# Kernel tuning notes

Hardware: AMD Instinct MI355X
Metric: run time of the kernel (lower is better)

The kernel has to match this reference:

```python
import jax, jax.numpy as jnp
import numpy as np

N_NODES = 100000
N_EDGES = 1250000
NUM_RELS = 8
D_IN, D_HID, D_OUT = 64, 64, 32


def setup_inputs() -> dict:
    key = jax.random.key(0)
    ks = jax.random.split(key, 10)
    x = jax.random.normal(ks[0], (N_NODES, D_IN), dtype=jnp.float32)
    src = jax.random.randint(ks[1], (N_EDGES,), 0, N_NODES, dtype=jnp.int32)
    dst = jax.random.randint(ks[2], (N_EDGES,), 0, N_NODES, dtype=jnp.int32)
    edge_type = jax.random.randint(ks[3], (N_EDGES,), 0, NUM_RELS, dtype=jnp.int32)
    s1 = 1.0 / np.sqrt(D_IN)
    s2 = 1.0 / np.sqrt(D_HID)
    W1 = jax.random.uniform(ks[4], (NUM_RELS, D_IN, D_HID), jnp.float32, -s1, s1)
    root1 = jax.random.uniform(ks[5], (D_IN, D_HID), jnp.float32, -s1, s1)
    b1 = jnp.zeros((D_HID,), jnp.float32)
    W2 = jax.random.uniform(ks[6], (NUM_RELS, D_HID, D_OUT), jnp.float32, -s2, s2)
    root2 = jax.random.uniform(ks[7], (D_HID, D_OUT), jnp.float32, -s2, s2)
    b2 = jnp.zeros((D_OUT,), jnp.float32)
    return {"x": x, "W1": W1, "root1": root1, "b1": b1,
            "W2": W2, "root2": root2, "b2": b2,
            "src": src, "dst": dst, "edge_type": edge_type}


def rgcn_conv(x, W, root, b, src, dst, edge_type, num_rels, num_nodes):
    # self-loop (root) transform + bias
    out = x @ root + b
    for r in range(num_rels):  # loop over small fixed relation set
        mask = (edge_type == r).astype(x.dtype)          # (E,)
        h = x @ W[r]                                      # (N, dout): transform once per relation
        msg = h[src] * mask[:, None]                      # (E, dout) gather + mask
        agg = jax.ops.segment_sum(msg, dst, num_segments=num_nodes)
        cnt = jax.ops.segment_sum(mask, dst, num_segments=num_nodes)
        out = out + agg / jnp.maximum(cnt, 1.0)[:, None]  # per-relation mean (PyG default aggr)
    return out


def reference(x, W1, root1, b1, W2, root2, b2, src, dst, edge_type):
    h = jax.nn.relu(rgcn_conv(x, W1, root1, b1, src, dst, edge_type, NUM_RELS, N_NODES))
    return rgcn_conv(h, W2, root2, b2, src, dst, edge_type, NUM_RELS, N_NODES)
```

## Files before the change

### kernel.cpp

```cpp
#include <hip/hip_runtime.h>

typedef _Float16 half8 __attribute__((ext_vector_type(8)));
typedef __attribute__((ext_vector_type(4))) float f32x4;

__device__ __forceinline__ unsigned short f2h(float f) {
    _Float16 h = (_Float16)f;
    return *(unsigned short*)&h;
}
__device__ __forceinline__ float h2f(unsigned short u) {
    _Float16 h = *(_Float16*)&u;
    return (float)h;
}


__device__ __forceinline__ void wprep_body(
    const float* __restrict__ W, const float* __restrict__ root,
    unsigned short* __restrict__ wb, int dout, int idx)
{
    int c = idx / (64 * dout);
    int rme = idx % (64 * dout);
    int kk = rme / dout;
    int j = rme % dout;
    float f = (c == 0) ? root[kk * dout + j]
                       : W[(size_t)(c - 1) * 64 * dout + kk * dout + j];
    wb[(size_t)c * dout * 72 + (size_t)j * 72 + kk] = f2h(f);
}

__global__ __launch_bounds__(256) void prep_kernel(
    const float* __restrict__ x, unsigned short* __restrict__ xh, int n8,
    const float* __restrict__ W1, const float* __restrict__ root1,
    unsigned short* __restrict__ wb1,
    const float* __restrict__ W2, const float* __restrict__ root2,
    unsigned short* __restrict__ wb2,
    int* __restrict__ hist, int nhist4)
{
    int id = blockIdx.x * 256 + threadIdx.x;
    if (id < n8) {
        const f32x4* p = (const f32x4*)(x + (size_t)id * 8);
        f32x4 u = p[0], v = p[1];
        half8 o;
#pragma unroll
        for (int j = 0; j < 4; ++j) {
            o[j] = (_Float16)u[j];
            o[j + 4] = (_Float16)v[j];
        }
        *(half8*)(xh + (size_t)id * 8) = o;
        return;
    }
    id -= n8;
    if (id < 9 * 64 * 64) { wprep_body(W1, root1, wb1, 64, id); return; }
    id -= 9 * 64 * 64;
    if (id < 9 * 64 * 32) { wprep_body(W2, root2, wb2, 32, id); return; }
    id -= 9 * 64 * 32;
    if (id < nhist4) ((int4*)hist)[id] = make_int4(0, 0, 0, 0);
}


__global__ __launch_bounds__(256) void hist8_kernel(
    const int* __restrict__ dst, const int* __restrict__ et,
    int* __restrict__ hist, int* __restrict__ rank, int E)
{
    int e = blockIdx.x * 256 + threadIdx.x;
    if (e < E) rank[e] = atomicAdd(&hist[dst[e] * 8 + et[e]], 1);
}

#define SCAN_TILE 4096
__global__ __launch_bounds__(1024) void scanA_kernel(
    const int* __restrict__ hist, int* __restrict__ bstart,
    int* __restrict__ partial, int nkeys)
{
    __shared__ int wsum[16];
    const int t = threadIdx.x;
    const int lane = t & 63, w = t >> 6;
    const int base = blockIdx.x * SCAN_TILE + t * 4;
    int v[4];
    int s = 0;
#pragma unroll
    for (int i = 0; i < 4; ++i) {
        v[i] = (base + i < nkeys) ? hist[base + i] : 0;
        s += v[i];
    }
    int inc = s;
#pragma unroll
    for (int off = 1; off < 64; off <<= 1) {
        int u = __shfl_up(inc, off);
        if (lane >= off) inc += u;
    }
    if (lane == 63) wsum[w] = inc;
    __syncthreads();
    if (w == 0 && lane < 16) {
        int ws = wsum[lane];
        int winc = ws;
#pragma unroll
        for (int off = 1; off < 16; off <<= 1) {
            int u = __shfl_up(winc, off);
            if (lane >= off) winc += u;
        }
        wsum[lane] = winc - ws;
    }
    __syncthreads();
    int run = wsum[w] + (inc - s);
    int tbase = run;
#pragma unroll
    for (int i = 0; i < 4; ++i) {
        if (base + i < nkeys) bstart[base + i] = run;
        run += v[i];
    }
    if (t == 1023) partial[blockIdx.x] = tbase + s;
}

__global__ __launch_bounds__(64) void scanB_kernel(
    const int* __restrict__ partial, int* __restrict__ pscan,
    int* __restrict__ bstart_end, int nblk)
{
    const int lane = threadIdx.x;
    int running = 0;
    for (int b = 0; b < nblk; b += 64) {
        int i = b + lane;
        int o = (i < nblk) ? partial[i] : 0;
        int v = o;
#pragma unroll
        for (int off = 1; off < 64; off <<= 1) {
            int u = __shfl_up(v, off);
            if (lane >= off) v += u;
        }
        if (i < nblk) pscan[i] = running + v - o;
        running += __shfl(v, 63);
    }
    if (lane == 0) *bstart_end = running;
}

__global__ __launch_bounds__(1024) void scanC_kernel(
    int* __restrict__ bstart, const int* __restrict__ pscan, int nkeys)
{
    int i = blockIdx.x * 1024 + threadIdx.x;
    if (i < nkeys) bstart[i] += pscan[i / SCAN_TILE];
}

__global__ __launch_bounds__(256) void scatter_kernel(
    const int* __restrict__ src, const int* __restrict__ dst,
    const int* __restrict__ et, const int* __restrict__ rank,
    const int* __restrict__ bstart, unsigned* __restrict__ srt, int E)
{
    int e = blockIdx.x * 256 + threadIdx.x;
    if (e < E) {
        int key = dst[e] * 8 + et[e];
        srt[bstart[key] + rank[e]] = (unsigned)src[e];
    }
}


template <int DOUT, int RELU, int OUTH>
__global__ __launch_bounds__(256, 6) void fused_kernel(
    const unsigned short* __restrict__ tab,
    const unsigned* __restrict__ srt,
    const int* __restrict__ bstart,
    const unsigned short* __restrict__ wb,
    const float* __restrict__ bias,
    float* __restrict__ outf,
    unsigned short* __restrict__ outh,
    int n_nodes)
{
    __shared__ __align__(16) unsigned short Atile[16 * 600];

    const int t = threadIdx.x;
    const int w = t >> 6, lane = t & 63;
    const int quad = lane >> 4, l16 = lane & 15;
    const int nb16 = blockIdx.x * 16;
    const int nb4 = nb16 + w * 4;
    const int KEYS = n_nodes * 8;

    {
        const int nb0 = nb4 * 8;
        int idx = nb0 + lane; if (idx > KEYS) idx = KEYS;
        const int myb = bstart[idx];
        const int blast = __builtin_amdgcn_readlane(myb, 32);
        const int E0 = __builtin_amdgcn_readlane(myb, 0);
        const int E1 = blast;

        int cnt = __shfl_down(myb, 1) - myb;
        float rsc = 1.0f / fmaxf((float)cnt, 1.0f);

#pragma unroll
        for (int i = 0; i < 4; ++i) {
            int node = nb4 + i;
            unsigned short v = 0;
            if (node < n_nodes) v = tab[(size_t)node * 64 + lane];
            Atile[(w * 4 + i) * 600 + lane] = v;
        }

        float acc = 0.f;
        int R = 0;
        int bnext = __builtin_amdgcn_readlane(myb, 1);

        auto flushes = [&](int eabs) {
            while (R < 32 && eabs == bnext) {
                float sc = __uint_as_float(
                    __builtin_amdgcn_readlane(__float_as_uint(rsc), R));
                Atile[(w * 4 + (R >> 3)) * 600 + 64 + (R & 7) * 64 + lane] =
                    f2h(acc * sc);
                acc = 0.f;
                ++R;
                bnext = (R < 31) ? __builtin_amdgcn_readlane(myb, R + 1) : blast;
            }
        };

        int base = E0;
        unsigned rec = 0;
        if (base < E1 && lane < E1 - base) rec = srt[base + lane];
        while (base < E1) {
            const int blen = min(64, E1 - base);
            const int nbase = base + 64;
            unsigned recn = 0;
            if (nbase < E1 && lane < E1 - nbase) recn = srt[nbase + lane];

            int k = 0;
            for (; k + 8 <= blen; k += 8) {
                unsigned q0 = (unsigned)__builtin_amdgcn_readlane((int)rec, k);
                unsigned q1 = (unsigned)__builtin_amdgcn_readlane((int)rec, k + 1);
                unsigned q2 = (unsigned)__builtin_amdgcn_readlane((int)rec, k + 2);
                unsigned q3 = (unsigned)__builtin_amdgcn_readlane((int)rec, k + 3);
                unsigned q4 = (unsigned)__builtin_amdgcn_readlane((int)rec, k + 4);
                unsigned q5 = (unsigned)__builtin_amdgcn_readlane((int)rec, k + 5);
                unsigned q6 = (unsigned)__builtin_amdgcn_readlane((int)rec, k + 6);
                unsigned q7 = (unsigned)__builtin_amdgcn_readlane((int)rec, k + 7);
                float v0 = h2f(tab[(size_t)q0 * 64 + lane]);
                float v1 = h2f(tab[(size_t)q1 * 64 + lane]);
                float v2 = h2f(tab[(size_t)q2 * 64 + lane]);
                float v3 = h2f(tab[(size_t)q3 * 64 + lane]);
                float v4 = h2f(tab[(size_t)q4 * 64 + lane]);
                float v5 = h2f(tab[(size_t)q5 * 64 + lane]);
                float v6 = h2f(tab[(size_t)q6 * 64 + lane]);
                float v7 = h2f(tab[(size_t)q7 * 64 + lane]);
                flushes(base + k);     acc += v0;
                flushes(base + k + 1); acc += v1;
                flushes(base + k + 2); acc += v2;
                flushes(base + k + 3); acc += v3;
                flushes(base + k + 4); acc += v4;
                flushes(base + k + 5); acc += v5;
                flushes(base + k + 6); acc += v6;
                flushes(base + k + 7); acc += v7;
            }
            for (; k < blen; ++k) {
                unsigned q = (unsigned)__builtin_amdgcn_readlane((int)rec, k);
                float v = h2f(tab[(size_t)q * 64 + lane]);
                flushes(base + k);
                acc += v;
            }
            base = nbase;
            rec = recn;
        }
        flushes(E1);
        while (R < 32) {
            float sc = __uint_as_float(
                __builtin_amdgcn_readlane(__float_as_uint(rsc), R));
            Atile[(w * 4 + (R >> 3)) * 600 + 64 + (R & 7) * 64 + lane] =
                f2h(acc * sc);
            acc = 0.f;
            ++R;
        }
    }

    __syncthreads();

    constexpr int JPW = DOUT / 16;
    if (JPW == 2 && w >= 2) return;

    const int j = w * 16 + l16;
    f32x4 d = {0.f, 0.f, 0.f, 0.f};
    const unsigned short* arow = &Atile[l16 * 600];
#pragma unroll
    for (int c = 0; c < 9; ++c) {
        half8 a0 = *(const half8*)(arow + c * 64 + quad * 8);
        half8 a1 = *(const half8*)(arow + c * 64 + 32 + quad * 8);
        half8 b0 = *(const half8*)&wb[c * DOUT * 72 + j * 72 + quad * 8];
        half8 b1 = *(const half8*)&wb[c * DOUT * 72 + j * 72 + 32 + quad * 8];
        d = __builtin_amdgcn_mfma_f32_16x16x32_f16(a0, b0, d, 0, 0, 0);
        d = __builtin_amdgcn_mfma_f32_16x16x32_f16(a1, b1, d, 0, 0, 0);
    }

    const float bj = bias[j];
#pragma unroll
    for (int r = 0; r < 4; ++r) {
        const int node = nb16 + quad * 4 + r;
        if (node < n_nodes) {
            float v = d[r] + bj;
            if (RELU) v = fmaxf(v, 0.0f);
            if (OUTH) outh[(size_t)node * 64 + j] = f2h(v);
            else      outf[(size_t)node * DOUT + j] = v;
        }
    }
}

extern "C" void kernel_launch(void* const* d_in, const int* in_sizes, int n_in,
                              void* d_out, int out_size, void* d_ws, size_t ws_size,
                              hipStream_t stream) {
    const float* x     = (const float*)d_in[0];
    const float* W1    = (const float*)d_in[1];
    const float* root1 = (const float*)d_in[2];
    const float* b1    = (const float*)d_in[3];
    const float* W2    = (const float*)d_in[4];
    const float* root2 = (const float*)d_in[5];
    const float* b2    = (const float*)d_in[6];
    const int*   src   = (const int*)d_in[7];
    const int*   dst   = (const int*)d_in[8];
    const int*   et    = (const int*)d_in[9];

    const int N = in_sizes[0] / 64;
    const int E = in_sizes[7];
    const int KEYS = N * 8;

    char* p = (char*)d_ws;
    auto alloc = [&](size_t bytes) {
        char* r = p;
        p += (bytes + 15) & ~(size_t)15;
        return r;
    };
    unsigned* srt       = (unsigned*)alloc((size_t)E * 4);
    int* rank           = (int*)alloc((size_t)E * 4);
    int* hist           = (int*)alloc((size_t)KEYS * 4);
    int* bstart         = (int*)alloc((size_t)(KEYS + 1) * 4);
    int* partial        = (int*)alloc(256 * 4);
    int* pscan          = (int*)alloc(256 * 4);
    unsigned short* wb1 = (unsigned short*)alloc((size_t)9 * 64 * 72 * 2);
    unsigned short* wb2 = (unsigned short*)alloc((size_t)9 * 32 * 72 * 2);
    unsigned short* xh  = (unsigned short*)alloc((size_t)N * 64 * 2);
    unsigned short* h   = (unsigned short*)alloc((size_t)N * 64 * 2);

    const int n8 = N * 8;
    const int nhist4 = KEYS / 4;
    const int prep_items = n8 + 9 * 64 * 64 + 9 * 64 * 32 + nhist4;
    prep_kernel<<<(prep_items + 255) / 256, 256, 0, stream>>>(
        x, xh, n8, W1, root1, wb1, W2, root2, wb2, hist, nhist4);

    hist8_kernel<<<(E + 255) / 256, 256, 0, stream>>>(dst, et, hist, rank, E);
    const int nscan = (KEYS + SCAN_TILE - 1) / SCAN_TILE;
    scanA_kernel<<<nscan, 1024, 0, stream>>>(hist, bstart, partial, KEYS);
    scanB_kernel<<<1, 64, 0, stream>>>(partial, pscan, bstart + KEYS, nscan);
    scanC_kernel<<<(KEYS + 1023) / 1024, 1024, 0, stream>>>(bstart, pscan, KEYS);
    scatter_kernel<<<(E + 255) / 256, 256, 0, stream>>>(src, dst, et, rank, bstart, srt, E);

    fused_kernel<64, 1, 1><<<(N + 15) / 16, 256, 0, stream>>>(
        xh, srt, bstart, wb1, b1, nullptr, h, N);
    fused_kernel<32, 0, 0><<<(N + 15) / 16, 256, 0, stream>>>(
        h, srt, bstart, wb2, b2, (float*)d_out, nullptr, N);
}
```

Before: 315.3 us.

## Fold scan fixup into consumers and double-buffer gather loads in fused kernel

Removes the scanC pass by adding the per-tile prefix offset (pscan[key>>12]) on the fly in the scatter and fused kernels. The fused kernel's gather loop now prefetches the next 16 neighbor rows into a second register buffer while it accumulates the current 16. It also splits the sum into two accumulators to shorten the dependent add chain. This saves one kernel launch and a full pass over bstart, and gives more memory-level parallelism in the gather, at the cost of extra registers and an extra pscan load per key read.

```diff
diff --git a/kernel.cpp b/kernel.cpp
--- a/kernel.cpp
+++ b/kernel.cpp
@@ -100,13 +100,12 @@
     }
     __syncthreads();
     int run = wsum[w] + (inc - s);
-    int tbase = run;
 #pragma unroll
     for (int i = 0; i < 4; ++i) {
         if (base + i < nkeys) bstart[base + i] = run;
         run += v[i];
     }
-    if (t == 1023) partial[blockIdx.x] = tbase + s;
+    if (t == 1023) partial[blockIdx.x] = run;
 }
 
 __global__ __launch_bounds__(64) void scanB_kernel(
@@ -130,22 +129,16 @@
     if (lane == 0) *bstart_end = running;
 }
 
-__global__ __launch_bounds__(1024) void scanC_kernel(
-    int* __restrict__ bstart, const int* __restrict__ pscan, int nkeys)
-{
-    int i = blockIdx.x * 1024 + threadIdx.x;
-    if (i < nkeys) bstart[i] += pscan[i / SCAN_TILE];
-}
-
 __global__ __launch_bounds__(256) void scatter_kernel(
     const int* __restrict__ src, const int* __restrict__ dst,
     const int* __restrict__ et, const int* __restrict__ rank,
-    const int* __restrict__ bstart, unsigned* __restrict__ srt, int E)
+    const int* __restrict__ bstart, const int* __restrict__ pscan,
+    unsigned* __restrict__ srt, int E)
 {
     int e = blockIdx.x * 256 + threadIdx.x;
     if (e < E) {
         int key = dst[e] * 8 + et[e];
-        srt[bstart[key] + rank[e]] = (unsigned)src[e];
+        srt[bstart[key] + pscan[key >> 12] + rank[e]] = (unsigned)src[e];
     }
 }
 
@@ -155,31 +148,33 @@
     const unsigned short* __restrict__ tab,
     const unsigned* __restrict__ srt,
     const int* __restrict__ bstart,
+    const int* __restrict__ pscan,
     const unsigned short* __restrict__ wb,
     const float* __restrict__ bias,
     float* __restrict__ outf,
     unsigned short* __restrict__ outh,
-    int n_nodes)
+    int n_nodes, int Etot)
 {
     __shared__ __align__(16) unsigned short Atile[16 * 600];
 
     const int t = threadIdx.x;
     const int w = t >> 6, lane = t & 63;
     const int quad = lane >> 4, l16 = lane & 15;
-    const int nb16 = blockIdx.x * 16;
-    const int nb4 = nb16 + w * 4;
+    const int nbt = blockIdx.x * 16;
+    const int nb4 = nbt + w * 4;
     const int KEYS = n_nodes * 8;
 
     {
         const int nb0 = nb4 * 8;
         int idx = nb0 + lane; if (idx > KEYS) idx = KEYS;
-        const int myb = bstart[idx];
-        const int blast = __builtin_amdgcn_readlane(myb, 32);
-        const int E0 = __builtin_amdgcn_readlane(myb, 0);
-        const int E1 = blast;
-
-        int cnt = __shfl_down(myb, 1) - myb;
-        float rsc = 1.0f / fmaxf((float)cnt, 1.0f);
+        int lv;
+        if (idx < KEYS) lv = bstart[idx] + pscan[idx >> 12];
+        else            lv = Etot;
+        const int E0 = __builtin_amdgcn_readlane(lv, 0);
+        const int E1 = __builtin_amdgcn_readlane(lv, 32);
+
+        int cntv = __shfl_down(lv, 1) - lv;
+        float rsc = 1.0f / fmaxf((float)cntv, 1.0f);
 
 #pragma unroll
         for (int i = 0; i < 4; ++i) {
@@ -189,21 +184,25 @@
             Atile[(w * 4 + i) * 600 + lane] = v;
         }
 
-        float acc = 0.f;
+        float acc0 = 0.f, acc1 = 0.f;
         int R = 0;
-        int bnext = __builtin_amdgcn_readlane(myb, 1);
+        int bnext = __builtin_amdgcn_readlane(lv, 1);
 
         auto flushes = [&](int eabs) {
             while (R < 32 && eabs == bnext) {
                 float sc = __uint_as_float(
                     __builtin_amdgcn_readlane(__float_as_uint(rsc), R));
                 Atile[(w * 4 + (R >> 3)) * 600 + 64 + (R & 7) * 64 + lane] =
-                    f2h(acc * sc);
-                acc = 0.f;
+                    f2h((acc0 + acc1) * sc);
+                acc0 = 0.f; acc1 = 0.f;
                 ++R;
-                bnext = (R < 31) ? __builtin_amdgcn_readlane(myb, R + 1) : blast;
+                bnext = (R < 31) ? __builtin_amdgcn_readlane(lv, R + 1) : E1;
             }
         };
+
+        const char* tabc = (const char*)tab;
+        const unsigned loff = (unsigned)(lane << 1);
+        unsigned short GA[16], GB[16];
 
         int base = E0;
         unsigned rec = 0;
@@ -214,49 +213,52 @@
             unsigned recn = 0;
             if (nbase < E1 && lane < E1 - nbase) recn = srt[nbase + lane];
 
-            int k = 0;
-            for (; k + 8 <= blen; k += 8) {
-                unsigned q0 = (unsigned)__builtin_amdgcn_readlane((int)rec, k);
-                unsigned q1 = (unsigned)__builtin_amdgcn_readlane((int)rec, k + 1);
-                unsigned q2 = (unsigned)__builtin_amdgcn_readlane((int)rec, k + 2);
-                unsigned q3 = (unsigned)__builtin_amdgcn_readlane((int)rec, k + 3);
-                unsigned q4 = (unsigned)__builtin_amdgcn_readlane((int)rec, k + 4);
-                unsigned q5 = (unsigned)__builtin_amdgcn_readlane((int)rec, k + 5);
-                unsigned q6 = (unsigned)__builtin_amdgcn_readlane((int)rec, k + 6);
-                unsigned q7 = (unsigned)__builtin_amdgcn_readlane((int)rec, k + 7);
-                float v0 = h2f(tab[(size_t)q0 * 64 + lane]);
-                float v1 = h2f(tab[(size_t)q1 * 64 + lane]);
-                float v2 = h2f(tab[(size_t)q2 * 64 + lane]);
-                float v3 = h2f(tab[(size_t)q3 * 64 + lane]);
-                float v4 = h2f(tab[(size_t)q4 * 64 + lane]);
-                float v5 = h2f(tab[(size_t)q5 * 64 + lane]);
-                float v6 = h2f(tab[(size_t)q6 * 64 + lane]);
-                float v7 = h2f(tab[(size_t)q7 * 64 + lane]);
-                flushes(base + k);     acc += v0;
-                flushes(base + k + 1); acc += v1;
-                flushes(base + k + 2); acc += v2;
-                flushes(base + k + 3); acc += v3;
-                flushes(base + k + 4); acc += v4;
-                flushes(base + k + 5); acc += v5;
-                flushes(base + k + 6); acc += v6;
-                flushes(base + k + 7); acc += v7;
+#pragma unroll
+            for (int i = 0; i < 16; ++i) {
+                unsigned q = (unsigned)__builtin_amdgcn_readlane((int)rec, i);
+                GA[i] = *(const unsigned short*)(tabc + ((size_t)q << 7) + loff);
             }
-            for (; k < blen; ++k) {
-                unsigned q = (unsigned)__builtin_amdgcn_readlane((int)rec, k);
-                float v = h2f(tab[(size_t)q * 64 + lane]);
-                flushes(base + k);
-                acc += v;
+            for (int b = 0; b < blen; b += 16) {
+                if (b + 16 < blen) {
+#pragma unroll
+                    for (int i = 0; i < 16; ++i) {
+                        unsigned q = (unsigned)__builtin_amdgcn_readlane(
+                            (int)rec, b + 16 + i);
+                        GB[i] = *(const unsigned short*)(
+                            tabc + ((size_t)q << 7) + loff);
+                    }
+                }
+                if (b + 16 <= blen) {
+#pragma unroll
+                    for (int i = 0; i < 16; ++i) {
+                        flushes(base + b + i);
+                        if (i & 1) acc1 += h2f(GA[i]);
+                        else       acc0 += h2f(GA[i]);
+                    }
+                } else {
+#pragma unroll
+                    for (int i = 0; i < 16; ++i) {
+                        if (b + i < blen) {
+                            flushes(base + b + i);
+                            if (i & 1) acc1 += h2f(GA[i]);
+                            else       acc0 += h2f(GA[i]);
+                        }
+                    }
+                }
+                if (b + 16 < blen) {
+#pragma unroll
+                    for (int i = 0; i < 16; ++i) GA[i] = GB[i];
+                }
             }
-            base = nbase;
-            rec = recn;
+            base = nbase; rec = recn;
         }
         flushes(E1);
         while (R < 32) {
             float sc = __uint_as_float(
                 __builtin_amdgcn_readlane(__float_as_uint(rsc), R));
             Atile[(w * 4 + (R >> 3)) * 600 + 64 + (R & 7) * 64 + lane] =
-                f2h(acc * sc);
-            acc = 0.f;
+                f2h((acc0 + acc1) * sc);
+            acc0 = 0.f; acc1 = 0.f;
             ++R;
         }
     }
@@ -282,7 +284,7 @@
     const float bj = bias[j];
 #pragma unroll
     for (int r = 0; r < 4; ++r) {
-        const int node = nb16 + quad * 4 + r;
+        const int node = nbt + quad * 4 + r;
         if (node < n_nodes) {
             float v = d[r] + bj;
             if (RELU) v = fmaxf(v, 0.0f);
@@ -337,11 +339,11 @@
     const int nscan = (KEYS + SCAN_TILE - 1) / SCAN_TILE;
     scanA_kernel<<<nscan, 1024, 0, stream>>>(hist, bstart, partial, KEYS);
     scanB_kernel<<<1, 64, 0, stream>>>(partial, pscan, bstart + KEYS, nscan);
-    scanC_kernel<<<(KEYS + 1023) / 1024, 1024, 0, stream>>>(bstart, pscan, KEYS);
-    scatter_kernel<<<(E + 255) / 256, 256, 0, stream>>>(src, dst, et, rank, bstart, srt, E);
+    scatter_kernel<<<(E + 255) / 256, 256, 0, stream>>>(
+        src, dst, et, rank, bstart, pscan, srt, E);
 
     fused_kernel<64, 1, 1><<<(N + 15) / 16, 256, 0, stream>>>(
-        xh, srt, bstart, wb1, b1, nullptr, h, N);
+        xh, srt, bstart, pscan, wb1, b1, nullptr, h, N, E);
     fused_kernel<32, 0, 0><<<(N + 15) / 16, 256, 0, stream>>>(
-        h, srt, bstart, wb2, b2, (float*)d_out, nullptr, N);
-}
+        h, srt, bstart, pscan, wb2, b2, (float*)d_out, nullptr, N, E);
+}
```

Measured after the change: 315.2 us. No clear change (-0.0%).
